# Optimization experiments

Hardware: AMD Instinct MI355X
Metric: run time of the kernel (lower is better)

## Reference

```python
import jax, jax.numpy as jnp
import numpy as np

DN = ('NCHW', 'OIHW', 'NCHW')

def conv(x, w, b, stride=1, pad=1):
    y = jax.lax.conv_general_dilated(x, w, (stride, stride), [(pad, pad), (pad, pad)], dimension_numbers=DN)
    return y + b[None, :, None, None]

def conv_t(x, w, b):
    # torch ConvTranspose2d(k=4, s=2, p=1): implemented as lhs-dilated conv, pad = k-1-p = 2
    y = jax.lax.conv_general_dilated(x, w, (1, 1), [(2, 2), (2, 2)], lhs_dilation=(2, 2), dimension_numbers=DN)
    return y + b[None, :, None, None]

def residual_stack(x, rw3, rb3, rw1, rb1):
    # canonical VQ-VAE residual block: x + conv1x1(relu(conv3x3(relu(x)))), then final relu
    n = rw3.shape[0]
    for i in range(n):
        h = conv(jax.nn.relu(x), rw3[i], rb3[i], 1, 1)
        h = conv(jax.nn.relu(h), rw1[i], rb1[i], 1, 0)
        x = x + h
    return jax.nn.relu(x)

def vq(x, codebook, beta):
    # x: [N, D, H, W] -> [N, H, W, D]
    x = jnp.transpose(x, (0, 2, 3, 1))
    shp = x.shape
    xf = x.reshape(-1, shp[-1])                               # [T, D]
    d = (jnp.sum(xf * xf, 1, keepdims=True)
         + jnp.sum(codebook * codebook, 1)
         - 2.0 * xf @ codebook.T)                             # [T, K]
    idx = jnp.argmin(d, axis=1)                               # [T]
    enc = jax.nn.one_hot(idx, codebook.shape[0], dtype=x.dtype)
    q = jnp.take(codebook, idx, axis=0).reshape(shp)
    loss_e = jnp.mean((jax.lax.stop_gradient(q) - x) ** 2)
    loss_q = jnp.mean((q - jax.lax.stop_gradient(x)) ** 2)
    loss = loss_q + beta * loss_e
    q_st = x + jax.lax.stop_gradient(q - x)
    p = jnp.mean(enc, axis=0)
    perplexity = jnp.exp(-jnp.sum(p * jnp.log(p + 1e-10)))
    return loss, jnp.transpose(q_st, (0, 3, 1, 2)), perplexity, enc

def setup_inputs() -> dict:
    key = jax.random.key(0)
    ks = jax.random.split(key, 24)
    C_img, C, RH, NR, K, D = 3, 128, 32, 2, 512, 64
    def g(k, shape, fan_in):
        return jax.random.normal(k, shape, jnp.float32) * (1.0 / np.sqrt(fan_in))
    inp = {
        'x': jax.random.normal(ks[0], (16, C_img, 256, 256), jnp.float32),
        'enc_w1': g(ks[1], (C // 2, C_img, 4, 4), C_img * 16), 'enc_b1': jnp.zeros((C // 2,)),
        'enc_w2': g(ks[2], (C, C // 2, 4, 4), C // 2 * 16), 'enc_b2': jnp.zeros((C,)),
        'enc_w3': g(ks[3], (C, C, 3, 3), C * 9), 'enc_b3': jnp.zeros((C,)),
        'enc_rw3': g(ks[4], (NR, RH, C, 3, 3), C * 9), 'enc_rb3': jnp.zeros((NR, RH)),
        'enc_rw1': g(ks[5], (NR, C, RH, 1, 1), RH), 'enc_rb1': jnp.zeros((NR, C)),
        'pre_w': g(ks[6], (D, C, 1, 1), C), 'pre_b': jnp.zeros((D,)),
        'codebook': jax.random.uniform(ks[7], (K, D), jnp.float32, -1.0 / K, 1.0 / K),
        'dec_w1': g(ks[8], (C, D, 3, 3), D * 9), 'dec_b1': jnp.zeros((C,)),
        'dec_rw3': g(ks[9], (NR, RH, C, 3, 3), C * 9), 'dec_rb3': jnp.zeros((NR, RH)),
        'dec_rw1': g(ks[10], (NR, C, RH, 1, 1), RH), 'dec_rb1': jnp.zeros((NR, C)),
        'dec_dw1': g(ks[11], (C // 2, C, 4, 4), C * 16), 'dec_db1': jnp.zeros((C // 2,)),
        'dec_dw2': g(ks[12], (C_img, C // 2, 4, 4), C // 2 * 16), 'dec_db2': jnp.zeros((C_img,)),
    }
    return inp

def reference(x, enc_w1, enc_b1, enc_w2, enc_b2, enc_w3, enc_b3, enc_rw3, enc_rb3, enc_rw1, enc_rb1,
              pre_w, pre_b, codebook, dec_w1, dec_b1, dec_rw3, dec_rb3, dec_rw1, dec_rb1,
              dec_dw1, dec_db1, dec_dw2, dec_db2):
    beta = 0.25
    # encoder
    h = jax.nn.relu(conv(x, enc_w1, enc_b1, 2, 1))
    h = jax.nn.relu(conv(h, enc_w2, enc_b2, 2, 1))
    h = conv(h, enc_w3, enc_b3, 1, 1)
    h = residual_stack(h, enc_rw3, enc_rb3, enc_rw1, enc_rb1)
    # pre-VQ 1x1 conv
    z = conv(h, pre_w, pre_b, 1, 0)
    # vector quantization
    loss, q, perplexity, _ = vq(z, codebook, beta)
    # decoder
    d = conv(q, dec_w1, dec_b1, 1, 1)
    d = residual_stack(d, dec_rw3, dec_rb3, dec_rw1, dec_rb1)
    d = jax.nn.relu(conv_t(d, dec_dw1, dec_db1))
    x_recon = conv_t(d, dec_dw2, dec_db2)
    return loss, x_recon, perplexity
```

## Files before the change

kernel.cpp:

```cpp
#include <hip/hip_runtime.h>

typedef __attribute__((ext_vector_type(8)))  short bf16x8;
typedef __attribute__((ext_vector_type(16))) float f32x16;
typedef unsigned long long u64t;

__device__ __forceinline__ int swzu(int u)
{
    return u ^ (((u >> 3) & 1) | (((u >> 4) & 1) << 1));
}

__device__ __forceinline__ void fsplit(float v, unsigned short& h, unsigned short& l)
{
    union { float f; unsigned u; } a; a.f = v;
    unsigned uh = a.u + 0x7fffu + ((a.u >> 16) & 1u);
    h = (unsigned short)(uh >> 16);
    union { float f; unsigned u; } hb; hb.u = (unsigned)h << 16;
    float r = v - hb.f;
    union { float f; unsigned u; } b; b.f = r;
    unsigned ul = b.u + 0x7fffu + ((b.u >> 16) & 1u);
    l = (unsigned short)(ul >> 16);
}

__device__ __forceinline__ float bf2f(unsigned short u)
{
    union { float f; unsigned v; } a; a.v = (unsigned)u << 16; return a.f;
}

struct PackDesc {
    const float* w;
    unsigned short *hi, *lo;
    int Co, Ci, KK, CoP, CiP;
    int blk0;
};
struct PackAll { PackDesc d[16]; int nd; };

__global__ __launch_bounds__(256) void pack_all(PackAll pa)
{
    int bx = blockIdx.x;
    int di = 0;
#pragma unroll
    for (int i = 0; i < 16; i++)
        if (i < pa.nd && bx >= pa.d[i].blk0) di = i;
    const PackDesc& D = pa.d[di];
    int i = (bx - D.blk0) * 256 + threadIdx.x;
    int tot = D.KK * D.CoP * D.CiP;
    if (i >= tot) return;
    int t  = i / (D.CoP * D.CiP);
    int r  = i - t * (D.CoP * D.CiP);
    int co = r / D.CiP;
    int ci = r - co * D.CiP;
    float v = (co < D.Co && ci < D.Ci) ? D.w[((size_t)co * D.Ci + ci) * D.KK + t] : 0.f;
    unsigned short h, l;
    fsplit(v, h, l);
    D.hi[i] = h; D.lo[i] = l;
}

__global__ __launch_bounds__(256) void vq_prep(const float* __restrict__ cb,
                                               float* __restrict__ cn, int* __restrict__ hist)
{
    int i = blockIdx.x * 256 + threadIdx.x;
    if (i < 512) {
        hist[i] = 0;
        float s = 0.f;
        for (int d = 0; d < 64; d++) s = fmaf(cb[i*64+d], cb[i*64+d], s);
        cn[i] = s;
    }
}

__global__ __launch_bounds__(256) void pack_x(const float* __restrict__ x,
    unsigned short* __restrict__ PH)
{
    int idx = blockIdx.x * 256 + threadIdx.x;
    int n = idx >> 16, pix = idx & 65535;
    unsigned short h[8], l[8];
#pragma unroll
    for (int c = 0; c < 8; c++) h[c] = 0;
#pragma unroll
    for (int c = 0; c < 3; c++) {
        float v = x[((size_t)(n * 3 + c) << 16) + pix];
        fsplit(v, h[c], l[c]);
    }
    uint4 hv;
    hv.x = h[0] | ((unsigned)h[1] << 16); hv.y = h[2] | ((unsigned)h[3] << 16);
    hv.z = h[4] | ((unsigned)h[5] << 16); hv.w = h[6] | ((unsigned)h[7] << 16);
    uint4 z4 = make_uint4(0, 0, 0, 0);
    size_t b0 = (((size_t)(n * 2) << 16) + pix) * 8;
    size_t b1 = (((size_t)(n * 2 + 1) << 16) + pix) * 8;
    *(uint4*)(PH + b0) = hv;
    *(uint4*)(PH + b1) = z4;
}

template<int K,int S,int P,int CIP,int COUT,int HIN,int WIN,int HOUT,int WOUT,
         int TR,int TC,int WM,int WN,int PX2,int CO2,int CC,int CO_PAD,
         bool PACK,bool PRELU,bool PLO,bool WF32,bool ROUT,bool RES>
__global__ __launch_bounds__(256) void conv_mfma(
    const unsigned short* __restrict__ inH,
    const unsigned short* __restrict__ wpH,
    const float* __restrict__ bias, const float* __restrict__ res,
    float* __restrict__ outF, unsigned short* __restrict__ outPH,
    unsigned short* __restrict__ outPL)
{
    constexpr int IHT = (TR - 1) * S + K;
    constexpr int IW  = (TC - 1) * S + K;
    constexpr int PS  = IHT * IW;
    constexpr int PLN = CC * 2;
    constexpr int UN  = PS * PLN;
    constexpr int KK  = K * K;
    constexpr int NCH = CIP / (CC * 16);
    constexpr int CG  = CIP / 8;
    constexpr int CGO = (COUT + 7) / 8;
    constexpr int XB  = WOUT / TC;
    constexpr int REGU = (UN + 255) / 256;
    constexpr int NST = CC * KK;

    __shared__ uint4 lbH[UN];

    const int tid = threadIdx.x;
    const int bx  = blockIdx.x;
    const int r0  = (bx / XB) * TR;
    const int c0  = (bx % XB) * TC;
    const int co0 = blockIdx.y * (WM * CO2 * 32);
    const int n   = blockIdx.z;

    const int l  = tid & 63, wv = tid >> 6;
    const int wm = wv / WN, wn = wv % WN;
    const int ln = l & 31, kg = l >> 5;

    int pb[PX2], gyv[PX2], gxv[PX2];
#pragma unroll
    for (int p2 = 0; p2 < PX2; p2++) {
        int q = wn * (PX2 * 32) + p2 * 32 + ln;
        int lr = q / TC, lc = q % TC;
        pb[p2] = (lr * S) * IW + lc * S;
        gyv[p2] = r0 + lr; gxv[p2] = c0 + lc;
    }

    const int iy0 = r0 * S - P, ix0 = c0 * S - P;
    const size_t inb = (size_t)n * CG * HIN * WIN;

    f32x16 acc[PX2][CO2];
#pragma unroll
    for (int p2 = 0; p2 < PX2; p2++)
#pragma unroll
        for (int g = 0; g < CO2; g++) acc[p2][g] = (f32x16){};

    auto unit_load = [&](int u, int cgb, uint4& hv){
        int kgu = u / PS, pos = u - kgu * PS;
        int py = pos / IW, px = pos - py * IW;
        int gy = iy0 + py, gx = ix0 + px;
        bool ok = ((unsigned)gy < (unsigned)HIN) && ((unsigned)gx < (unsigned)WIN);
        hv = make_uint4(0,0,0,0);
        if (ok) {
            size_t a = (inb + ((size_t)(cgb + kgu) * HIN + gy) * WIN + gx) * 8;
            hv = *(const uint4*)(inH + a);
        }
    };

    auto stage_direct = [&](int kc){
        for (int idx = tid; idx < UN; idx += 256) {
            uint4 hv;
            unit_load(idx, kc * PLN, hv);
            lbH[swzu(idx)] = hv;
        }
    };

    uint4 rvH[REGU];
    auto load_regs = [&](int kc){
#pragma unroll
        for (int rr = 0; rr < REGU; rr++) {
            int idx = tid + rr * 256;
            uint4 hv = make_uint4(0,0,0,0);
            if (idx < UN) unit_load(idx, kc * PLN, hv);
            rvH[rr] = hv;
        }
    };
    auto write_regs = [&](){
#pragma unroll
        for (int rr = 0; rr < REGU; rr++) {
            int idx = tid + rr * 256;
            if (idx < UN) lbH[swzu(idx)] = rvH[rr];
        }
    };

    auto compute = [&](int kc){
        bf16x8 aC[CO2], aN[CO2], bC[PX2], bN[PX2];
        auto loadA = [&](int step, bf16x8* a){
            const int ks = step / KK, t = step - ks * KK;
#pragma unroll
            for (int g = 0; g < CO2; g++) {
                const int coA = co0 + (wm * CO2 + g) * 32 + ln;
                const size_t wo = ((size_t)t * CO_PAD + coA) * CIP
                                + kc * (CC * 16) + ks * 16 + kg * 8;
                a[g] = *(const bf16x8*)(wpH + wo);
            }
        };
        auto loadB = [&](int step, bf16x8* b){
            const int ks = step / KK, t = step - ks * KK;
            const int ky = t / K, kx = t - ky * K;
#pragma unroll
            for (int p2 = 0; p2 < PX2; p2++) {
                const int u = (ks * 2 + kg) * PS + pb[p2] + ky * IW + kx;
                b[p2] = *(const bf16x8*)&lbH[swzu(u)];
            }
        };
        loadA(0, aC); loadB(0, bC);
#pragma unroll
        for (int step = 0; step < NST; step++) {
            if (step + 1 < NST) { loadA(step + 1, aN); loadB(step + 1, bN); }
#pragma unroll
            for (int p2 = 0; p2 < PX2; p2++)
#pragma unroll
                for (int g = 0; g < CO2; g++)
                    acc[p2][g] = __builtin_amdgcn_mfma_f32_32x32x16_bf16(
                        aC[g], bC[p2], acc[p2][g], 0, 0, 0);
            if (step + 1 < NST) {
#pragma unroll
                for (int g = 0; g < CO2; g++) aC[g] = aN[g];
#pragma unroll
                for (int p2 = 0; p2 < PX2; p2++) bC[p2] = bN[p2];
            }
        }
    };

    stage_direct(0);
    __syncthreads();
    for (int kc = 0; kc < NCH; kc++) {
        const bool more = (kc + 1 < NCH);
        if (more) load_regs(kc + 1);
        compute(kc);
        if (more) {
            __syncthreads();
            write_regs();
            __syncthreads();
        }
    }

    const size_t HWo = (size_t)HOUT * WOUT;
#pragma unroll
    for (int p2 = 0; p2 < PX2; p2++) {
        const int gy = gyv[p2], gx = gxv[p2];
#pragma unroll
        for (int g = 0; g < CO2; g++) {
            const int co32 = co0 + (wm * CO2 + g) * 32;
#pragma unroll
            for (int rq = 0; rq < 4; rq++) {
                const int cb4 = co32 + 8 * rq + 4 * kg;
                float v[4];
#pragma unroll
                for (int i = 0; i < 4; i++) {
                    const int r = rq * 4 + i;
                    const int co = cb4 + i;
                    float bv = (co < COUT) ? bias[co] : 0.f;
                    float vv = acc[p2][g][r] + bv;
                    if (RES && co < COUT)
                        vv += res[((size_t)n * COUT + co) * HWo + (size_t)gy * WOUT + gx];
                    if (ROUT) vv = fmaxf(vv, 0.f);
                    if (WF32 && co < COUT)
                        outF[((size_t)n * COUT + co) * HWo + (size_t)gy * WOUT + gx] = vv;
                    v[i] = vv;
                }
                if (PACK) {
                    u64t uh = 0, ul = 0;
#pragma unroll
                    for (int i = 0; i < 4; i++) {
                        float pv = PRELU ? fmaxf(v[i], 0.f) : v[i];
                        unsigned short ph, pl;
                        fsplit(pv, ph, pl);
                        uh |= (u64t)ph << (16 * i);
                        ul |= (u64t)pl << (16 * i);
                    }
                    size_t pa = (((size_t)n * CGO + (co32 >> 3) + rq) * HOUT + gy) * (size_t)WOUT * 8
                              + (size_t)gx * 8 + 4 * kg;
                    *(u64t*)(outPH + pa) = uh;
                    if (PLO) *(u64t*)(outPL + pa) = ul;
                }
            }
        }
    }
}

__global__ __launch_bounds__(256) void fused_res(
    const unsigned short* __restrict__ inH,
    const unsigned short* __restrict__ w3H,
    const float* __restrict__ b3,
    const unsigned short* __restrict__ w1H,
    const float* __restrict__ b1,
    float* __restrict__ Cf,
    unsigned short* __restrict__ outPH)
{
    constexpr int H = 64, W = 64;
    constexpr int IHT = 4, IW = 66, PS = IHT * IW;
    constexpr int CC = 2, PLN = 4, UN = PS * PLN;
    constexpr int NCH = 4, NST = 18;
    constexpr int REGU = (UN + 255) / 256;
    constexpr int CG = 16, CGO = 16;

    __shared__ uint4 lbH[UN];
    __shared__ unsigned short midL[4 * 128 * 8];

    const int tid = threadIdx.x;
    const int r0  = blockIdx.x * 2;
    const int n   = blockIdx.z;
    const int l  = tid & 63, wv = tid >> 6;
    const int ln = l & 31, kg = l >> 5;

    const int pxl1 = wv * 32 + ln;
    const int lr1 = pxl1 / W, lc1 = pxl1 % W;
    const int pb1 = lr1 * IW + lc1;

    const int iy0 = r0 - 1, ix0 = -1;
    const size_t inb = (size_t)n * CG * H * W;

    auto unit_load = [&](int u, int cgb, uint4& hv){
        int kgu = u / PS, pos = u - kgu * PS;
        int py = pos / IW, px = pos - py * IW;
        int gy = iy0 + py, gx = ix0 + px;
        bool ok = ((unsigned)gy < (unsigned)H) && ((unsigned)gx < (unsigned)W);
        hv = make_uint4(0,0,0,0);
        if (ok) {
            size_t a = (inb + ((size_t)(cgb + kgu) * H + gy) * W + gx) * 8;
            hv = *(const uint4*)(inH + a);
        }
    };
    auto stage_direct = [&](int kc){
        for (int idx = tid; idx < UN; idx += 256) {
            uint4 hv;
            unit_load(idx, kc * PLN, hv);
            lbH[swzu(idx)] = hv;
        }
    };
    uint4 rvH[REGU];
    auto load_regs = [&](int kc){
#pragma unroll
        for (int rr = 0; rr < REGU; rr++) {
            int idx = tid + rr * 256;
            uint4 hv = make_uint4(0,0,0,0);
            if (idx < UN) unit_load(idx, kc * PLN, hv);
            rvH[rr] = hv;
        }
    };
    auto write_regs = [&](){
#pragma unroll
        for (int rr = 0; rr < REGU; rr++) {
            int idx = tid + rr * 256;
            if (idx < UN) lbH[swzu(idx)] = rvH[rr];
        }
    };

    f32x16 acc1 = {};
    auto compute = [&](int kc){
        bf16x8 aC, aN, bC, bN;
        auto loadA = [&](int step, bf16x8& a){
            const int ks = step / 9, t = step - ks * 9;
            a = *(const bf16x8*)(w3H + ((size_t)t * 32 + ln) * 128
                                 + kc * 32 + ks * 16 + kg * 8);
        };
        auto loadB = [&](int step, bf16x8& b){
            const int ks = step / 9, t = step - ks * 9;
            const int ky = t / 3, kx = t - ky * 3;
            const int u = (ks * 2 + kg) * PS + pb1 + ky * IW + kx;
            b = *(const bf16x8*)&lbH[swzu(u)];
        };
        loadA(0, aC); loadB(0, bC);
#pragma unroll
        for (int step = 0; step < NST; step++) {
            if (step + 1 < NST) { loadA(step + 1, aN); loadB(step + 1, bN); }
            acc1 = __builtin_amdgcn_mfma_f32_32x32x16_bf16(aC, bC, acc1, 0, 0, 0);
            if (step + 1 < NST) { aC = aN; bC = bN; }
        }
    };

    stage_direct(0);
    __syncthreads();
    for (int kc = 0; kc < NCH; kc++) {
        const bool more = (kc + 1 < NCH);
        if (more) load_regs(kc + 1);
        compute(kc);
        if (more) {
            __syncthreads();
            write_regs();
            __syncthreads();
        }
    }

#pragma unroll
    for (int r = 0; r < 16; r++) {
        const int co = (r & 3) + 8 * (r >> 2) + 4 * kg;
        float vv = fmaxf(acc1[r] + b3[co], 0.f);
        unsigned short h, lo_;
        fsplit(vv, h, lo_);
        midL[((co >> 3) * 128 + pxl1) * 8 + (co & 7)] = h;
    }
    __syncthreads();

    f32x16 acc2[4];
#pragma unroll
    for (int pg = 0; pg < 4; pg++) acc2[pg] = (f32x16){};
#pragma unroll
    for (int pg = 0; pg < 4; pg++) {
#pragma unroll
        for (int ks = 0; ks < 2; ks++) {
            bf16x8 b = *(const bf16x8*)&midL[((ks * 2 + kg) * 128 + pg * 32 + ln) * 8];
            bf16x8 a = *(const bf16x8*)(w1H + ((size_t)(wv * 32 + ln)) * 32
                                        + ks * 16 + kg * 8);
            acc2[pg] = __builtin_amdgcn_mfma_f32_32x32x16_bf16(a, b, acc2[pg], 0, 0, 0);
        }
    }

    const int co32 = wv * 32;
#pragma unroll
    for (int pg = 0; pg < 4; pg++) {
        const int pxl = pg * 32 + ln;
        const int gy = r0 + pxl / W, gx = pxl % W;
#pragma unroll
        for (int rq = 0; rq < 4; rq++) {
            const int cb4 = co32 + 8 * rq + 4 * kg;
            float v[4];
#pragma unroll
            for (int i = 0; i < 4; i++) {
                const int r = rq * 4 + i;
                const int co = cb4 + i;
                size_t ra = ((size_t)n * 128 + co) * (H * W) + (size_t)gy * W + gx;
                float vv = acc2[pg][r] + b1[co] + Cf[ra];
                Cf[ra] = vv;
                v[i] = vv;
            }
            u64t uh = 0;
#pragma unroll
            for (int i = 0; i < 4; i++) {
                float pv = fmaxf(v[i], 0.f);
                unsigned short ph, pl;
                fsplit(pv, ph, pl);
                uh |= (u64t)ph << (16 * i);
            }
            size_t pa = (((size_t)n * CGO + (co32 >> 3) + rq) * H + gy) * (size_t)W * 8
                      + (size_t)gx * 8 + 4 * kg;
            *(u64t*)(outPH + pa) = uh;
        }
    }
}

template<int CIP,int COUT,int HW,int CO_PAD,
         bool PACK,bool PRELU,bool PLO,bool WF32,bool ROUT,bool RES>
__global__ __launch_bounds__(256) void conv1x1_mfma(
    const unsigned short* __restrict__ inH,
    const unsigned short* __restrict__ wpH,
    const float* __restrict__ bias, const float* __restrict__ res,
    float* __restrict__ outF, unsigned short* __restrict__ outPH,
    unsigned short* __restrict__ outPL)
{
    constexpr int NCH = CIP / 16;
    constexpr int CG  = CIP / 8;
    constexpr int CGO = (COUT + 7) / 8;

    const int tid = threadIdx.x;
    const int bx  = blockIdx.x;
    const int co0 = blockIdx.y * 64;
    const int n   = blockIdx.z;

    const int l  = tid & 63, wv = tid >> 6;
    const int wm = wv >> 1, wn = wv & 1;
    const int ln = l & 31, kg = l >> 5;

    const int pix = bx * 64 + wn * 32 + ln;
    const int coA = co0 + wm * 32 + ln;

    f32x16 acc = {};
#pragma unroll
    for (int kc = 0; kc < NCH; kc++) {
        bf16x8 b = *(const bf16x8*)(inH + ((size_t)(n * CG + kc * 2 + kg) * HW + pix) * 8);
        bf16x8 a = *(const bf16x8*)(wpH + ((size_t)coA * CIP + kc * 16 + kg * 8));
        acc = __builtin_amdgcn_mfma_f32_32x32x16_bf16(a, b, acc, 0, 0, 0);
    }

    const int co32 = co0 + wm * 32;
#pragma unroll
    for (int rq = 0; rq < 4; rq++) {
        const int cb4 = co32 + 8 * rq + 4 * kg;
        float v[4];
#pragma unroll
        for (int i = 0; i < 4; i++) {
            const int r = rq * 4 + i;
            const int co = cb4 + i;
            float bv = (co < COUT) ? bias[co] : 0.f;
            float vv = acc[r] + bv;
            if (RES && co < COUT)
                vv += res[((size_t)n * COUT + co) * HW + pix];
            if (ROUT) vv = fmaxf(vv, 0.f);
            if (WF32 && co < COUT)
                outF[((size_t)n * COUT + co) * HW + pix] = vv;
            v[i] = vv;
        }
        if (PACK) {
            u64t uh = 0, ul = 0;
#pragma unroll
            for (int i = 0; i < 4; i++) {
                float pv = PRELU ? fmaxf(v[i], 0.f) : v[i];
                unsigned short ph, pl;
                fsplit(pv, ph, pl);
                uh |= (u64t)ph << (16 * i);
                ul |= (u64t)pl << (16 * i);
            }
            size_t pa = (((size_t)n * CGO + (co32 >> 3) + rq) * HW + pix) * 8 + 4 * kg;
            *(u64t*)(outPH + pa) = uh;
            if (PLO) *(u64t*)(outPL + pa) = ul;
        }
    }
}

template<int CIP,int COUT,int HIN,int WIN,int CO2,int CC,int CO_PAD,
         bool PACK,bool WF32,bool ROUT>
__global__ __launch_bounds__(256) void convt_mfma(
    const unsigned short* __restrict__ inH,
    const unsigned short* __restrict__ wpH,
    const float* __restrict__ bias, float* __restrict__ outF,
    unsigned short* __restrict__ outPH)
{
    constexpr int HOUT = 2 * HIN, WOUT = 2 * WIN;
    constexpr int XHN  = WOUT / 128;
    constexpr int PS   = 3 * 68;
    constexpr int PLN  = CC * 2;
    constexpr int UN   = PS * PLN;
    constexpr int NCH  = CIP / (CC * 16);
    constexpr int CG   = CIP / 8;
    constexpr int CGO  = (COUT + 7) / 8;
    constexpr int REGU = (UN + 255) / 256;
    constexpr int NST  = CC * 4;

    __shared__ uint4 lbH[UN];

    const int tid = threadIdx.x;
    const int xh  = blockIdx.x % XHN;
    const int gr  = blockIdx.x / XHN;
    const int oy0 = (gr >> 1) * 4 + (gr & 1);
    const int co0 = blockIdx.y * (CO2 * 32);
    const int n   = blockIdx.z;

    const int ky0 = oy0 & 1;
    const int iyb = ((oy0 + ky0) >> 1) - 1;

    const int l  = tid & 63, wv = tid >> 6;
    const int pw = wv & 1, xb = wv >> 1;
    const int ln = l & 31, kg = l >> 5;

    const size_t inb = (size_t)n * CG * HIN * WIN;

    f32x16 acc[2][CO2];
#pragma unroll
    for (int r2 = 0; r2 < 2; r2++)
#pragma unroll
        for (int g = 0; g < CO2; g++) acc[r2][g] = (f32x16){};

    auto unit_load = [&](int u, int cgb, uint4& hv){
        int kgu = u / PS, pos = u - kgu * PS;
        int rr = pos / 68, cc = pos - rr * 68;
        int gy = iyb + rr, gx = xh * 64 + cc - 1;
        bool ok = ((unsigned)gy < (unsigned)HIN) && ((unsigned)gx < (unsigned)WIN);
        hv = make_uint4(0,0,0,0);
        if (ok) {
            size_t a = (inb + ((size_t)(cgb + kgu) * HIN + gy) * WIN + gx) * 8;
            hv = *(const uint4*)(inH + a);
        }
    };

    auto stage_direct = [&](int kc){
        for (int idx = tid; idx < UN; idx += 256) {
            uint4 hv;
            unit_load(idx, kc * PLN, hv);
            lbH[swzu(idx)] = hv;
        }
    };

    uint4 rvH[REGU];
    auto load_regs = [&](int kc){
#pragma unroll
        for (int rr = 0; rr < REGU; rr++) {
            int idx = tid + rr * 256;
            uint4 hv = make_uint4(0,0,0,0);
            if (idx < UN) unit_load(idx, kc * PLN, hv);
            rvH[rr] = hv;
        }
    };
    auto write_regs = [&](){
#pragma unroll
        for (int rr = 0; rr < REGU; rr++) {
            int idx = tid + rr * 256;
            if (idx < UN) lbH[swzu(idx)] = rvH[rr];
        }
    };

    auto compute = [&](int kc){
        bf16x8 aC[CO2], aN[CO2], bC[2], bN[2];
        auto loadA = [&](int step, bf16x8* a){
            const int ks = step / 4, tt = step - ks * 4;
            const int widx = (ky0 + 2 * (tt >> 1)) * 4 + (pw + 2 * (tt & 1));
#pragma unroll
            for (int g = 0; g < CO2; g++) {
                const int coA = co0 + g * 32 + ln;
                const size_t wo = ((size_t)widx * CO_PAD + coA) * CIP
                                + kc * (CC * 16) + ks * 16 + kg * 8;
                a[g] = *(const bf16x8*)(wpH + wo);
            }
        };
        auto loadB = [&](int step, bf16x8* bv){
            const int ks = step / 4, tt = step - ks * 4;
            const int ty = tt >> 1, tx = tt & 1;
#pragma unroll
            for (int r2 = 0; r2 < 2; r2++) {
                const int u = (ks * 2 + kg) * PS + (r2 + ty) * 68 + xb * 32 + ln + pw + tx;
                bv[r2] = *(const bf16x8*)&lbH[swzu(u)];
            }
        };
        loadA(0, aC); loadB(0, bC);
#pragma unroll
        for (int step = 0; step < NST; step++) {
            if (step + 1 < NST) { loadA(step + 1, aN); loadB(step + 1, bN); }
#pragma unroll
            for (int r2 = 0; r2 < 2; r2++)
#pragma unroll
                for (int g = 0; g < CO2; g++)
                    acc[r2][g] = __builtin_amdgcn_mfma_f32_32x32x16_bf16(
                        aC[g], bC[r2], acc[r2][g], 0, 0, 0);
            if (step + 1 < NST) {
#pragma unroll
                for (int g = 0; g < CO2; g++) aC[g] = aN[g];
#pragma unroll
                for (int r2 = 0; r2 < 2; r2++) bC[r2] = bN[r2];
            }
        }
    };

    stage_direct(0);
    __syncthreads();
    for (int kc = 0; kc < NCH; kc++) {
        const bool more = (kc + 1 < NCH);
        if (more) load_regs(kc + 1);
        compute(kc);
        if (more) {
            __syncthreads();
            write_regs();
            __syncthreads();
        }
    }

    const int ox = xh * 128 + pw + 2 * (xb * 32 + ln);
    const size_t HWo = (size_t)HOUT * WOUT;
#pragma unroll
    for (int r2 = 0; r2 < 2; r2++) {
        const int oy = oy0 + 2 * r2;
#pragma unroll
        for (int g = 0; g < CO2; g++) {
            const int co32 = co0 + g * 32;
#pragma unroll
            for (int rq = 0; rq < 4; rq++) {
                const int cb4 = co32 + 8 * rq + 4 * kg;
                float v[4];
#pragma unroll
                for (int i = 0; i < 4; i++) {
                    const int r = rq * 4 + i;
                    const int co = cb4 + i;
                    float bv = (co < COUT) ? bias[co] : 0.f;
                    float vv = acc[r2][g][r] + bv;
                    if (ROUT) vv = fmaxf(vv, 0.f);
                    if (WF32 && co < COUT)
                        outF[((size_t)n * COUT + co) * HWo + (size_t)oy * WOUT + ox] = vv;
                    v[i] = vv;
                }
                if (PACK) {
                    u64t uh = 0;
#pragma unroll
                    for (int i = 0; i < 4; i++) {
                        unsigned short ph, pl;
                        fsplit(v[i], ph, pl);
                        uh |= (u64t)ph << (16 * i);
                    }
                    size_t pa = (((size_t)n * CGO + (co32 >> 3) + rq) * HOUT + oy) * (size_t)WOUT * 8
                              + (size_t)ox * 8 + 4 * kg;
                    *(u64t*)(outPH + pa) = uh;
                }
            }
        }
    }
}

__global__ __launch_bounds__(256) void vq_mfma(
    const unsigned short* __restrict__ zPH, const unsigned short* __restrict__ zPL,
    const unsigned short* __restrict__ cbH, const unsigned short* __restrict__ cbL,
    const float* __restrict__ cnorm,
    unsigned short* __restrict__ qPH,
    float* __restrict__ ssep, int* __restrict__ hist)
{
    __shared__ unsigned short zH[128 * 72];
    __shared__ unsigned short zL[128 * 72];
    __shared__ float cnl[512];
    __shared__ int   hl[512];

    const int tid = threadIdx.x;
    const int blk = blockIdx.x;

    for (int i = tid; i < 512; i += 256) { cnl[i] = cnorm[i]; hl[i] = 0; }

    for (int idx = tid; idx < 1024; idx += 256) {
        int tok = idx >> 3, cg = idx & 7;
        int t = blk * 128 + tok;
        int n = t >> 12, pix = t & 4095;
        size_t a = (((size_t)(n * 8 + cg)) * 4096 + pix) * 8;
        *(uint4*)&zH[tok * 72 + cg * 8] = *(const uint4*)(zPH + a);
        *(uint4*)&zL[tok * 72 + cg * 8] = *(const uint4*)(zPL + a);
    }
    __syncthreads();

    const int l  = tid & 63, wv = tid >> 6;
    const int ln = l & 31, kg = l >> 5;
    const int tok = wv * 32 + ln;

    float xn = 0.f;
#pragma unroll
    for (int j8 = 0; j8 < 8; j8++) {
        bf16x8 vH = *(const bf16x8*)&zH[tok * 72 + j8 * 8];
        bf16x8 vL = *(const bf16x8*)&zL[tok * 72 + j8 * 8];
#pragma unroll
        for (int j = 0; j < 8; j++) {
            float xv = bf2f((unsigned short)vH[j]) + bf2f((unsigned short)vL[j]);
            xn = fmaf(xv, xv, xn);
        }
    }

    float bm = 3.4e38f; int bidx = 0;
    for (int cg = 0; cg < 16; cg++) {
        f32x16 a0 = {}, a1 = {};
#pragma unroll
        for (int ks = 0; ks < 4; ks++) {
            const size_t wo = ((size_t)(cg * 32 + ln)) * 64 + ks * 16 + kg * 8;
            bf16x8 aH = *(const bf16x8*)(cbH + wo);
            bf16x8 aL = *(const bf16x8*)(cbL + wo);
            bf16x8 bH = *(const bf16x8*)&zH[tok * 72 + ks * 16 + kg * 8];
            bf16x8 bL = *(const bf16x8*)&zL[tok * 72 + ks * 16 + kg * 8];
            a0 = __builtin_amdgcn_mfma_f32_32x32x16_bf16(aH, bH, a0, 0, 0, 0);
            a1 = __builtin_amdgcn_mfma_f32_32x32x16_bf16(aH, bL, a1, 0, 0, 0);
            a1 = __builtin_amdgcn_mfma_f32_32x32x16_bf16(aL, bH, a1, 0, 0, 0);
        }
#pragma unroll
        for (int r = 0; r < 16; r++) {
            int m    = (r & 3) + 8 * (r >> 2) + 4 * kg;
            int code = cg * 32 + m;
            float s  = a0[r] + a1[r];
            float dm = cnl[code] - 2.f * s;
            if (dm < bm) { bm = dm; bidx = code; }
        }
    }

    float bm2 = __shfl_xor(bm, 32);
    int   bi2 = __shfl_xor(bidx, 32);
    if (bm2 < bm || (bm2 == bm && bi2 < bidx)) { bm = bm2; bidx = bi2; }

    {
        int t = blk * 128 + tok;
        int n = t >> 12, pix = t & 4095;
#pragma unroll
        for (int cgl = 0; cgl < 4; cgl++) {
            int cg = kg * 4 + cgl;
            uint4 hv = *(const uint4*)(cbH + (size_t)bidx * 64 + cg * 8);
            size_t a = (((size_t)(n * 8 + cg)) * 4096 + pix) * 8;
            *(uint4*)(qPH + a) = hv;
        }
    }

    float bestd = xn + bm;
    float c = (kg == 0) ? bestd : 0.f;
#pragma unroll
    for (int o = 32; o > 0; o >>= 1) c += __shfl_down(c, o, 64);
    if (l == 0) ssep[blk * 4 + wv] = c;
    if (kg == 0) atomicAdd(&hl[bidx], 1);
    __syncthreads();
    for (int i = tid; i < 512; i += 256) if (hl[i] > 0) atomicAdd(&hist[i], hl[i]);
}

__global__ __launch_bounds__(256) void vq_finalize(
    const float* __restrict__ ssep, const int* __restrict__ hist,
    float* __restrict__ o_loss, float* __restrict__ o_perp)
{
    __shared__ float red[256];
    const int tid = threadIdx.x;
    float h = 0.f;
    for (int i = tid; i < 512; i += 256) {
        float p = (float)hist[i] * (1.0f / 65536.0f);
        h -= p * logf(p + 1e-10f);
    }
    red[tid] = h;
    __syncthreads();
    for (int st = 128; st > 0; st >>= 1) {
        if (tid < st) red[tid] += red[tid + st];
        __syncthreads();
    }
    const float H = red[0];
    __syncthreads();
    float s = 0.f;
    for (int i = tid; i < 2048; i += 256) s += ssep[i];
    red[tid] = s;
    __syncthreads();
    for (int st = 128; st > 0; st >>= 1) {
        if (tid < st) red[tid] += red[tid + st];
        __syncthreads();
    }
    if (tid == 0) {
        *o_loss = 1.25f * red[0] / 4194304.0f;
        *o_perp = expf(H);
    }
}

extern "C" void kernel_launch(void* const* d_in, const int* in_sizes, int n_in,
                              void* d_out, int out_size, void* d_ws, size_t ws_size,
                              hipStream_t stream)
{
    const float* x       = (const float*)d_in[0];
    const float* enc_w1  = (const float*)d_in[1];
    const float* enc_b1  = (const float*)d_in[2];
    const float* enc_w2  = (const float*)d_in[3];
    const float* enc_b2  = (const float*)d_in[4];
    const float* enc_w3  = (const float*)d_in[5];
    const float* enc_b3  = (const float*)d_in[6];
    const float* enc_rw3 = (const float*)d_in[7];
    const float* enc_rb3 = (const float*)d_in[8];
    const float* enc_rw1 = (const float*)d_in[9];
    const float* enc_rb1 = (const float*)d_in[10];
    const float* pre_w   = (const float*)d_in[11];
    const float* pre_b   = (const float*)d_in[12];
    const float* cb      = (const float*)d_in[13];
    const float* dec_w1  = (const float*)d_in[14];
    const float* dec_b1  = (const float*)d_in[15];
    const float* dec_rw3 = (const float*)d_in[16];
    const float* dec_rb3 = (const float*)d_in[17];
    const float* dec_rw1 = (const float*)d_in[18];
    const float* dec_rb1 = (const float*)d_in[19];
    const float* dw1     = (const float*)d_in[20];
    const float* db1     = (const float*)d_in[21];
    const float* dw2     = (const float*)d_in[22];
    const float* db2     = (const float*)d_in[23];

    float* o      = (float*)d_out;
    float* loss_p = o;
    float* recon  = o + 1;
    float* perp_p = o + 1 + 16 * 3 * 256 * 256;

    unsigned short* R1H = (unsigned short*)d_ws;
    unsigned short* R1L = R1H + 16777216;
    unsigned short* R2H = R1L + 16777216;
    unsigned short* R2L = R2H + 16777216;
    float* Cf  = (float*)(R2L + 16777216);
    float* SSE = Cf + 8388608;
    int*   HIST = (int*)(SSE + 2048);

    unsigned short *xPH = R1H;
    unsigned short *BPH = R1H;
    unsigned short *zPH = R1H + 8388608, *zPL = R1L + 8388608;
    unsigned short *dAPH = R1H;
    unsigned short *APH = R2H;
    unsigned short *C1PH = R2H;
    unsigned short *C2PH = R2L;
    unsigned short *qPH = R2H + 8388608;

    unsigned short* wp_cur = (unsigned short*)(((size_t)(HIST + 512) + 31) & ~(size_t)31);
    auto carve = [&](size_t n_us) {
        unsigned short* p = wp_cur;
        wp_cur += ((n_us + 15) & ~(size_t)15);
        return p;
    };

    unsigned short *e1H = carve(16*64*16),  *e1L = carve(16*64*16);
    unsigned short *e2H = carve(16*128*64), *e2L = carve(16*128*64);
    unsigned short *e3H = carve(9*128*128), *e3L = carve(9*128*128);
    unsigned short *er3aH = carve(9*32*128), *er3aL = carve(9*32*128);
    unsigned short *er3bH = carve(9*32*128), *er3bL = carve(9*32*128);
    unsigned short *er1aH = carve(128*32),   *er1aL = carve(128*32);
    unsigned short *er1bH = carve(128*32),   *er1bL = carve(128*32);
    unsigned short *preH = carve(64*128),    *preL = carve(64*128);
    unsigned short *d1H  = carve(9*128*64),  *d1L  = carve(9*128*64);
    unsigned short *dr3aH = carve(9*32*128), *dr3aL = carve(9*32*128);
    unsigned short *dr3bH = carve(9*32*128), *dr3bL = carve(9*32*128);
    unsigned short *dr1aH = carve(128*32),   *dr1aL = carve(128*32);
    unsigned short *dr1bH = carve(128*32),   *dr1bL = carve(128*32);
    unsigned short *ct1H = carve(16*64*128), *ct1L = carve(16*64*128);
    unsigned short *ct2H = carve(16*32*64),  *ct2L = carve(16*32*64);
    unsigned short *cbH  = carve(512*64),    *cbL  = carve(512*64);
    float* CN = (float*)carve(1024);

    PackAll pa; int nb = 0;
    auto addPK = [&](int i, const float* w, unsigned short* hi, unsigned short* lo,
                     int Co, int Ci, int KK, int CoP, int CiP) {
        pa.d[i] = {w, hi, lo, Co, Ci, KK, CoP, CiP, nb};
        nb += (KK * CoP * CiP + 255) / 256;
    };
    addPK(0,  enc_w1, e1H, e1L, 64, 3, 16, 64, 16);
    addPK(1,  enc_w2, e2H, e2L, 128, 64, 16, 128, 64);
    addPK(2,  enc_w3, e3H, e3L, 128, 128, 9, 128, 128);
    addPK(3,  enc_rw3,            er3aH, er3aL, 32, 128, 9, 32, 128);
    addPK(4,  enc_rw3 + 32*128*9, er3bH, er3bL, 32, 128, 9, 32, 128);
    addPK(5,  enc_rw1,            er1aH, er1aL, 128, 32, 1, 128, 32);
    addPK(6,  enc_rw1 + 128*32,   er1bH, er1bL, 128, 32, 1, 128, 32);
    addPK(7,  pre_w, preH, preL, 64, 128, 1, 64, 128);
    addPK(8,  dec_w1, d1H, d1L, 128, 64, 9, 128, 64);
    addPK(9,  dec_rw3,            dr3aH, dr3aL, 32, 128, 9, 32, 128);
    addPK(10, dec_rw3 + 32*128*9, dr3bH, dr3bL, 32, 128, 9, 32, 128);
    addPK(11, dec_rw1,            dr1aH, dr1aL, 128, 32, 1, 128, 32);
    addPK(12, dec_rw1 + 128*32,   dr1bH, dr1bL, 128, 32, 1, 128, 32);
    addPK(13, dw1, ct1H, ct1L, 64, 128, 16, 64, 128);
    addPK(14, dw2, ct2H, ct2L, 3, 64, 16, 32, 64);
    addPK(15, cb,  cbH,  cbL,  512, 64, 1, 512, 64);
    pa.nd = 16;
    pack_all<<<dim3(nb), dim3(256), 0, stream>>>(pa);
    vq_prep<<<dim3(2), dim3(256), 0, stream>>>(cb, CN, HIST);
    pack_x<<<dim3(4096), dim3(256), 0, stream>>>(x, xPH);

    const int N = 16;

    conv_mfma<4,2,1, 16,64, 256,256, 128,128, 2,64, 2,2,2,1, 1, 64,
              true,false,false,false,true,false>
        <<<dim3(128,1,N),256,0,stream>>>(xPH, e1H, enc_b1, nullptr, nullptr, APH, nullptr);
    conv_mfma<4,2,1, 64,128, 128,128, 64,64, 2,64, 2,2,2,2, 1, 128,
              true,false,false,false,true,false>
        <<<dim3(32,1,N),256,0,stream>>>(APH, e2H, enc_b2, nullptr, nullptr, BPH, nullptr);
    conv_mfma<3,1,1, 128,128, 64,64, 64,64, 2,64, 2,2,2,2, 2, 128,
              true,true,false,true,false,false>
        <<<dim3(32,1,N),256,0,stream>>>(BPH, e3H, enc_b3, nullptr, Cf, C1PH, nullptr);
    fused_res<<<dim3(32,1,N),256,0,stream>>>(C1PH, er3aH, enc_rb3, er1aH, enc_rb1, Cf, C2PH);
    fused_res<<<dim3(32,1,N),256,0,stream>>>(C2PH, er3bH, enc_rb3 + 32, er1bH, enc_rb1 + 128, Cf, C1PH);
    conv1x1_mfma<128,64, 4096, 64,   true,false,true,false,false,false>
        <<<dim3(64,1,N),256,0,stream>>>(C1PH, preH, pre_b, nullptr, nullptr, zPH, zPL);

    vq_mfma<<<dim3(512), dim3(256), 0, stream>>>(zPH, zPL, cbH, cbL, CN, qPH, SSE, HIST);
    vq_finalize<<<dim3(1), dim3(256), 0, stream>>>(SSE, HIST, loss_p, perp_p);

    conv_mfma<3,1,1, 64,128, 64,64, 64,64, 2,64, 2,2,2,2, 2, 128,
              true,true,false,true,false,false>
        <<<dim3(32,1,N),256,0,stream>>>(qPH, d1H, dec_b1, nullptr, Cf, C1PH, nullptr);
    fused_res<<<dim3(32,1,N),256,0,stream>>>(C1PH, dr3aH, dec_rb3, dr1aH, dec_rb1, Cf, C2PH);
    fused_res<<<dim3(32,1,N),256,0,stream>>>(C2PH, dr3bH, dec_rb3 + 32, dr1bH, dec_rb1 + 128, Cf, C1PH);
    convt_mfma<128,64, 64,64, 2, 2, 64,  true,false,true>
        <<<dim3(64,1,N),256,0,stream>>>(C1PH, ct1H, db1, nullptr, dAPH);
    convt_mfma<64,3, 128,128, 1, 2, 32,  false,true,false>
        <<<dim3(256,1,N),256,0,stream>>>(dAPH, ct2H, db2, recon, nullptr);
}
```

Before: 462.3 us.

## Fuse pre-VQ 1x1 conv into VQ kernel and gather codebook in decoder conv

The pre-VQ 1x1 convolution is computed inside the VQ kernel with MFMA directly from the packed encoder activations, so the intermediate z hi/lo tensors are never written to or read back from global memory. The VQ kernel now stores only a 16-bit code index per token instead of writing the quantized vectors. The first decoder conv gathers codebook rows through these indices while staging its input tile. This removes one launch and several large intermediate tensors, but the decoder conv does one dependent index load per staged unit, and the 1x1 conv work is repeated per VQ block rather than tiled separately.

```diff
diff --git a/kernel.cpp b/kernel.cpp
--- a/kernel.cpp
+++ b/kernel.cpp
@@ -92,13 +92,14 @@
 
 template<int K,int S,int P,int CIP,int COUT,int HIN,int WIN,int HOUT,int WOUT,
          int TR,int TC,int WM,int WN,int PX2,int CO2,int CC,int CO_PAD,
-         bool PACK,bool PRELU,bool PLO,bool WF32,bool ROUT,bool RES>
+         bool PACK,bool PRELU,bool PLO,bool WF32,bool ROUT,bool RES,bool GATHER>
 __global__ __launch_bounds__(256) void conv_mfma(
     const unsigned short* __restrict__ inH,
     const unsigned short* __restrict__ wpH,
     const float* __restrict__ bias, const float* __restrict__ res,
     float* __restrict__ outF, unsigned short* __restrict__ outPH,
-    unsigned short* __restrict__ outPL)
+    unsigned short* __restrict__ outPL,
+    const unsigned short* __restrict__ gcb, const unsigned short* __restrict__ gidx)
 {
     constexpr int IHT = (TR - 1) * S + K;
     constexpr int IW  = (TC - 1) * S + K;
@@ -151,8 +152,13 @@
         bool ok = ((unsigned)gy < (unsigned)HIN) && ((unsigned)gx < (unsigned)WIN);
         hv = make_uint4(0,0,0,0);
         if (ok) {
-            size_t a = (inb + ((size_t)(cgb + kgu) * HIN + gy) * WIN + gx) * 8;
-            hv = *(const uint4*)(inH + a);
+            if constexpr (GATHER) {
+                int id = gidx[(size_t)n * (HIN * WIN) + (size_t)gy * WIN + gx];
+                hv = *(const uint4*)(gcb + ((size_t)id * 64 + (size_t)(cgb + kgu) * 8));
+            } else {
+                size_t a = (inb + ((size_t)(cgb + kgu) * HIN + gy) * WIN + gx) * 8;
+                hv = *(const uint4*)(inH + a);
+            }
         }
     };
 
@@ -440,74 +446,6 @@
     }
 }
 
-template<int CIP,int COUT,int HW,int CO_PAD,
-         bool PACK,bool PRELU,bool PLO,bool WF32,bool ROUT,bool RES>
-__global__ __launch_bounds__(256) void conv1x1_mfma(
-    const unsigned short* __restrict__ inH,
-    const unsigned short* __restrict__ wpH,
-    const float* __restrict__ bias, const float* __restrict__ res,
-    float* __restrict__ outF, unsigned short* __restrict__ outPH,
-    unsigned short* __restrict__ outPL)
-{
-    constexpr int NCH = CIP / 16;
-    constexpr int CG  = CIP / 8;
-    constexpr int CGO = (COUT + 7) / 8;
-
-    const int tid = threadIdx.x;
-    const int bx  = blockIdx.x;
-    const int co0 = blockIdx.y * 64;
-    const int n   = blockIdx.z;
-
-    const int l  = tid & 63, wv = tid >> 6;
-    const int wm = wv >> 1, wn = wv & 1;
-    const int ln = l & 31, kg = l >> 5;
-
-    const int pix = bx * 64 + wn * 32 + ln;
-    const int coA = co0 + wm * 32 + ln;
-
-    f32x16 acc = {};
-#pragma unroll
-    for (int kc = 0; kc < NCH; kc++) {
-        bf16x8 b = *(const bf16x8*)(inH + ((size_t)(n * CG + kc * 2 + kg) * HW + pix) * 8);
-        bf16x8 a = *(const bf16x8*)(wpH + ((size_t)coA * CIP + kc * 16 + kg * 8));
-        acc = __builtin_amdgcn_mfma_f32_32x32x16_bf16(a, b, acc, 0, 0, 0);
-    }
-
-    const int co32 = co0 + wm * 32;
-#pragma unroll
-    for (int rq = 0; rq < 4; rq++) {
-        const int cb4 = co32 + 8 * rq + 4 * kg;
-        float v[4];
-#pragma unroll
-        for (int i = 0; i < 4; i++) {
-            const int r = rq * 4 + i;
-            const int co = cb4 + i;
-            float bv = (co < COUT) ? bias[co] : 0.f;
-            float vv = acc[r] + bv;
-            if (RES && co < COUT)
-                vv += res[((size_t)n * COUT + co) * HW + pix];
-            if (ROUT) vv = fmaxf(vv, 0.f);
-            if (WF32 && co < COUT)
-                outF[((size_t)n * COUT + co) * HW + pix] = vv;
-            v[i] = vv;
-        }
-        if (PACK) {
-            u64t uh = 0, ul = 0;
-#pragma unroll
-            for (int i = 0; i < 4; i++) {
-                float pv = PRELU ? fmaxf(v[i], 0.f) : v[i];
-                unsigned short ph, pl;
-                fsplit(pv, ph, pl);
-                uh |= (u64t)ph << (16 * i);
-                ul |= (u64t)pl << (16 * i);
-            }
-            size_t pa = (((size_t)n * CGO + (co32 >> 3) + rq) * HW + pix) * 8 + 4 * kg;
-            *(u64t*)(outPH + pa) = uh;
-            if (PLO) *(u64t*)(outPL + pa) = ul;
-        }
-    }
-}
-
 template<int CIP,int COUT,int HIN,int WIN,int CO2,int CC,int CO_PAD,
          bool PACK,bool WF32,bool ROUT>
 __global__ __launch_bounds__(256) void convt_mfma(
@@ -683,11 +621,13 @@
     }
 }
 
-__global__ __launch_bounds__(256) void vq_mfma(
-    const unsigned short* __restrict__ zPH, const unsigned short* __restrict__ zPL,
+__global__ __launch_bounds__(256) void vq_fused(
+    const unsigned short* __restrict__ C1PH,
+    const unsigned short* __restrict__ preH,
+    const float* __restrict__ pre_b,
     const unsigned short* __restrict__ cbH, const unsigned short* __restrict__ cbL,
     const float* __restrict__ cnorm,
-    unsigned short* __restrict__ qPH,
+    unsigned short* __restrict__ IDX,
     float* __restrict__ ssep, int* __restrict__ hist)
 {
     __shared__ unsigned short zH[128 * 72];
@@ -700,19 +640,36 @@
 
     for (int i = tid; i < 512; i += 256) { cnl[i] = cnorm[i]; hl[i] = 0; }
 
-    for (int idx = tid; idx < 1024; idx += 256) {
-        int tok = idx >> 3, cg = idx & 7;
-        int t = blk * 128 + tok;
-        int n = t >> 12, pix = t & 4095;
-        size_t a = (((size_t)(n * 8 + cg)) * 4096 + pix) * 8;
-        *(uint4*)&zH[tok * 72 + cg * 8] = *(const uint4*)(zPH + a);
-        *(uint4*)&zL[tok * 72 + cg * 8] = *(const uint4*)(zPL + a);
-    }
-    __syncthreads();
-
     const int l  = tid & 63, wv = tid >> 6;
     const int ln = l & 31, kg = l >> 5;
     const int tok = wv * 32 + ln;
+    const int t   = blk * 128 + tok;
+    const int n   = t >> 12, pix = t & 4095;
+
+    f32x16 az[2];
+    az[0] = (f32x16){}; az[1] = (f32x16){};
+#pragma unroll
+    for (int kc = 0; kc < 8; kc++) {
+        bf16x8 b = *(const bf16x8*)(C1PH + ((size_t)(n * 16 + kc * 2 + kg) * 4096 + pix) * 8);
+#pragma unroll
+        for (int g = 0; g < 2; g++) {
+            bf16x8 a = *(const bf16x8*)(preH + ((size_t)(g * 32 + ln)) * 128
+                                        + kc * 16 + kg * 8);
+            az[g] = __builtin_amdgcn_mfma_f32_32x32x16_bf16(a, b, az[g], 0, 0, 0);
+        }
+    }
+#pragma unroll
+    for (int g = 0; g < 2; g++)
+#pragma unroll
+        for (int r = 0; r < 16; r++) {
+            const int d = g * 32 + (r & 3) + 8 * (r >> 2) + 4 * kg;
+            float vv = az[g][r] + pre_b[d];
+            unsigned short h, lo_;
+            fsplit(vv, h, lo_);
+            zH[tok * 72 + d] = h;
+            zL[tok * 72 + d] = lo_;
+        }
+    __syncthreads();
 
     float xn = 0.f;
 #pragma unroll
@@ -754,17 +711,7 @@
     int   bi2 = __shfl_xor(bidx, 32);
     if (bm2 < bm || (bm2 == bm && bi2 < bidx)) { bm = bm2; bidx = bi2; }
 
-    {
-        int t = blk * 128 + tok;
-        int n = t >> 12, pix = t & 4095;
-#pragma unroll
-        for (int cgl = 0; cgl < 4; cgl++) {
-            int cg = kg * 4 + cgl;
-            uint4 hv = *(const uint4*)(cbH + (size_t)bidx * 64 + cg * 8);
-            size_t a = (((size_t)(n * 8 + cg)) * 4096 + pix) * 8;
-            *(uint4*)(qPH + a) = hv;
-        }
-    }
+    if (kg == 0) IDX[t] = (unsigned short)bidx;
 
     float bestd = xn + bm;
     float c = (kg == 0) ? bestd : 0.f;
@@ -850,17 +797,16 @@
     float* Cf  = (float*)(R2L + 16777216);
     float* SSE = Cf + 8388608;
     int*   HIST = (int*)(SSE + 2048);
+    unsigned short* IDXb = (unsigned short*)(HIST + 512);
 
     unsigned short *xPH = R1H;
     unsigned short *BPH = R1H;
-    unsigned short *zPH = R1H + 8388608, *zPL = R1L + 8388608;
     unsigned short *dAPH = R1H;
     unsigned short *APH = R2H;
     unsigned short *C1PH = R2H;
     unsigned short *C2PH = R2L;
-    unsigned short *qPH = R2H + 8388608;
-
-    unsigned short* wp_cur = (unsigned short*)(((size_t)(HIST + 512) + 31) & ~(size_t)31);
+
+    unsigned short* wp_cur = (unsigned short*)(((size_t)(IDXb + 65536) + 31) & ~(size_t)31);
     auto carve = [&](size_t n_us) {
         unsigned short* p = wp_cur;
         wp_cur += ((n_us + 15) & ~(size_t)15);
@@ -915,25 +861,28 @@
     const int N = 16;
 
     conv_mfma<4,2,1, 16,64, 256,256, 128,128, 2,64, 2,2,2,1, 1, 64,
-              true,false,false,false,true,false>
-        <<<dim3(128,1,N),256,0,stream>>>(xPH, e1H, enc_b1, nullptr, nullptr, APH, nullptr);
+              true,false,false,false,true,false,false>
+        <<<dim3(128,1,N),256,0,stream>>>(xPH, e1H, enc_b1, nullptr, nullptr, APH, nullptr,
+                                         nullptr, nullptr);
     conv_mfma<4,2,1, 64,128, 128,128, 64,64, 2,64, 2,2,2,2, 1, 128,
-              true,false,false,false,true,false>
-        <<<dim3(32,1,N),256,0,stream>>>(APH, e2H, enc_b2, nullptr, nullptr, BPH, nullptr);
+              true,false,false,false,true,false,false>
+        <<<dim3(32,1,N),256,0,stream>>>(APH, e2H, enc_b2, nullptr, nullptr, BPH, nullptr,
+                                        nullptr, nullptr);
     conv_mfma<3,1,1, 128,128, 64,64, 64,64, 2,64, 2,2,2,2, 2, 128,
-              true,true,false,true,false,false>
-        <<<dim3(32,1,N),256,0,stream>>>(BPH, e3H, enc_b3, nullptr, Cf, C1PH, nullptr);
+              true,true,false,true,false,false,false>
+        <<<dim3(32,1,N),256,0,stream>>>(BPH, e3H, enc_b3, nullptr, Cf, C1PH, nullptr,
+                                        nullptr, nullptr);
     fused_res<<<dim3(32,1,N),256,0,stream>>>(C1PH, er3aH, enc_rb3, er1aH, enc_rb1, Cf, C2PH);
     fused_res<<<dim3(32,1,N),256,0,stream>>>(C2PH, er3bH, enc_rb3 + 32, er1bH, enc_rb1 + 128, Cf, C1PH);
-    conv1x1_mfma<128,64, 4096, 64,   true,false,true,false,false,false>
-        <<<dim3(64,1,N),256,0,stream>>>(C1PH, preH, pre_b, nullptr, nullptr, zPH, zPL);
-
-    vq_mfma<<<dim3(512), dim3(256), 0, stream>>>(zPH, zPL, cbH, cbL, CN, qPH, SSE, HIST);
+
+    vq_fused<<<dim3(512), dim3(256), 0, stream>>>(C1PH, preH, pre_b, cbH, cbL, CN,
+                                                  IDXb, SSE, HIST);
     vq_finalize<<<dim3(1), dim3(256), 0, stream>>>(SSE, HIST, loss_p, perp_p);
 
     conv_mfma<3,1,1, 64,128, 64,64, 64,64, 2,64, 2,2,2,2, 2, 128,
-              true,true,false,true,false,false>
-        <<<dim3(32,1,N),256,0,stream>>>(qPH, d1H, dec_b1, nullptr, Cf, C1PH, nullptr);
+              true,true,false,true,false,false,true>
+        <<<dim3(32,1,N),256,0,stream>>>(nullptr, d1H, dec_b1, nullptr, Cf, C1PH, nullptr,
+                                        cbH, IDXb);
     fused_res<<<dim3(32,1,N),256,0,stream>>>(C1PH, dr3aH, dec_rb3, dr1aH, dec_rb1, Cf, C2PH);
     fused_res<<<dim3(32,1,N),256,0,stream>>>(C2PH, dr3bH, dec_rb3 + 32, dr1bH, dec_rb1 + 128, Cf, C1PH);
     convt_mfma<128,64, 64,64, 2, 2, 64,  true,false,true>
```

Result: no change. 453.5 us (-1.9%).
